# Kernel tuning notes

Measured on AMD Instinct MI355X. Metric: run time of the kernel, lower is better.

The kernel has to match this reference:

```python
import jax, jax.numpy as jnp
import numpy as np

B, D, V, E = 8192, 512, 64, 8
HIDDEN = (1024, 512, 256)


def _mlp_dims(d_in, d_out):
    dims = (d_in,) + HIDDEN + (d_out,)
    return list(zip(dims[:-1], dims[1:]))


def setup_inputs() -> dict:
    key = jax.random.key(0)
    ks = iter(jax.random.split(key, 64))
    inp = {
        'obs': jax.random.normal(next(ks), (B, D), dtype=jnp.float32),
        'code': jax.random.normal(next(ks), (B, V), dtype=jnp.float32),
    }
    # stacked expert MLP params: [E, d_in, d_out] / [E, d_out]
    for i, (di, do) in enumerate(_mlp_dims(D, 1)):
        s = 1.0 / np.sqrt(di)
        inp[f'ew{i}'] = jax.random.uniform(next(ks), (E, di, do), jnp.float32, -s, s)
        inp[f'eb{i}'] = jax.random.uniform(next(ks), (E, do), jnp.float32, -s, s)
    # gate MLP params: [d_in, d_out] / [d_out]
    for i, (di, do) in enumerate(_mlp_dims(V, E)):
        s = 1.0 / np.sqrt(di)
        inp[f'gw{i}'] = jax.random.uniform(next(ks), (di, do), jnp.float32, -s, s)
        inp[f'gb{i}'] = jax.random.uniform(next(ks), (do,), jnp.float32, -s, s)
    return inp


def reference(obs, code, ew0, eb0, ew1, eb1, ew2, eb2, ew3, eb3,
              gw0, gb0, gw1, gb1, gw2, gb2, gw3, gb3):
    # gate: MLP(num_vqvae -> hidden -> num_experts) + softmax
    g = code
    for w, b in ((gw0, gb0), (gw1, gb1), (gw2, gb2)):
        g = jax.nn.elu(g @ w + b)
    weights = jax.nn.softmax(g @ gw3 + gb3, axis=-1)  # [B, E]

    # experts: batched over E via einsum (replaces Python loop of 8 MLPs)
    h = obs  # [B, D] broadcast into [B, E, h]
    h = jax.nn.elu(jnp.einsum('bi,eio->beo', h, ew0) + eb0)
    h = jax.nn.elu(jnp.einsum('bei,eio->beo', h, ew1) + eb1)
    h = jax.nn.elu(jnp.einsum('bei,eio->beo', h, ew2) + eb2)
    returns = (jnp.einsum('bei,eio->beo', h, ew3) + eb3)[..., 0]  # [B, E]

    # bmm(weights[B,1,E], returns[B,E,1]).squeeze(-1) -> [B, 1]
    return jnp.sum(weights * returns, axis=-1, keepdims=True)
```

## Files before the change

### kernel.cpp

```cpp
#include <hip/hip_runtime.h>
#include <hip/hip_bf16.h>
#include <math.h>


typedef _Float16 f16x8 __attribute__((ext_vector_type(8)));
typedef float f32x4 __attribute__((ext_vector_type(4)));

#define AS1 __attribute__((address_space(1)))
#define AS3 __attribute__((address_space(3)))
#define SCHED0 __builtin_amdgcn_sched_barrier(0)
#define SBAR __builtin_amdgcn_s_barrier()

__device__ __forceinline__ ushort h2u(_Float16 h){
  union { _Float16 h; ushort u; } v; v.h = h; return v.u;
}
__device__ __forceinline__ float elu_f(float x){
  return x > 0.f ? x : __expf(x) - 1.f;
}

struct AJob { const float* X; ushort* A; int total; };
__global__ void prep_act_all(AJob j0, AJob j1, int t0){
  int i = blockIdx.x * 256 + threadIdx.x;
  AJob J; int idx;
  if (i < t0){ J = j0; idx = i; }
  else { J = j1; idx = i - t0; if (idx >= J.total) return; }
  J.A[idx] = h2u((_Float16)J.X[idx]);
}

struct WJob { const float* W; ushort* Bt; int K, N, nb, nk, blkStart; };
struct WJobs { WJob j[6]; int njobs; };
__global__ void prep_w_all(WJobs jobs){
  __shared__ float tile[32][33];
  int b = blockIdx.x;
  int ji = 0;
  while (ji + 1 < jobs.njobs && b >= jobs.j[ji + 1].blkStart) ji++;
  WJob J = jobs.j[ji];
  int rem = b - J.blkStart;
  int x = rem % J.nb; rem /= J.nb;
  int y = rem % J.nk; int e = rem / J.nk;
  const float* w = J.W + (size_t)e * J.K * J.N;
  ushort* bt = J.Bt + (size_t)e * J.N * J.K;
  int n0 = x * 32, k0 = y * 32;
  for (int i = threadIdx.y; i < 32; i += 8)
    tile[i][threadIdx.x] = w[(size_t)(k0 + i) * J.N + n0 + threadIdx.x];
  __syncthreads();
  for (int jj = threadIdx.y; jj < 32; jj += 8){
    float v = tile[threadIdx.x][jj];
    bt[(size_t)(n0 + jj) * J.K + k0 + threadIdx.x] = h2u((_Float16)v);
  }
}

struct Slice {
  const ushort* A; const ushort* Bt; const float* bias; void* C;
  const float* w3; const float* rbp; float* ret;
  int N, K, log2gx, mode, blkStart, eidx;
};
struct SliceArr { Slice s[9]; int nz; };

__global__ __launch_bounds__(256, 3) void gemm8p(SliceArr args){
  __shared__ __align__(16) ushort As[128][64];
  __shared__ __align__(16) ushort Bs[128][64];
  __shared__ float red[2][128];

  const int nwg  = gridDim.x;
  const int orig = blockIdx.x;
  const int wg   = (orig & 7) * (nwg >> 3) + (orig >> 3);

  int z = 0;
  while (z + 1 < args.nz && wg >= args.s[z + 1].blkStart) z++;
  const Slice sl = args.s[z];
  const int rem = wg - sl.blkStart;
  const int gxm = (1 << sl.log2gx) - 1;
  const int bx  = rem & gxm;
  const int by  = rem >> sl.log2gx;

  const ushort* __restrict__ Ag = sl.A;
  const ushort* __restrict__ Bg = sl.Bt;
  const int K = sl.K;

  const int tid  = threadIdx.x;
  const int lane = tid & 63;
  const int wave = tid >> 6;
  const int wr = wave >> 1;
  const int wc = wave & 1;
  const int rowBase = by * 128;
  const int colBase = bx * 128;
  const int KB = K >> 6;
  const int lr = lane & 15;
  const int lk = (lane >> 4) << 3;
  const int swzR = (lr & 7) << 3;

  const int rS = tid >> 3;
  const int cS = ((tid & 7) << 3) ^ ((rS & 7) << 3);

  auto stage = [&](int kt){
    int tt = (kt < KB) ? kt : (KB - 1);
    int kc = (tt << 6) + cS;
    {
      char* lb = (char*)&As[0][0];
      #pragma unroll
      for (int j = 0; j < 4; j++){
        const ushort* src = Ag + (size_t)(rowBase + j * 32 + rS) * (size_t)K + kc;
        __builtin_amdgcn_global_load_lds((const AS1 void*)src,
                                         (AS3 void*)(lb + j * 4096 + tid * 16), 16, 0, 0);
      }
    }
    {
      char* lb = (char*)&Bs[0][0];
      #pragma unroll
      for (int j = 0; j < 4; j++){
        const ushort* src = Bg + (size_t)(colBase + j * 32 + rS) * (size_t)K + kc;
        __builtin_amdgcn_global_load_lds((const AS1 void*)src,
                                         (AS3 void*)(lb + j * 4096 + tid * 16), 16, 0, 0);
      }
    }
  };

  f16x8 av[4], bv[4];
  auto readKs = [&](int ks){
    int kc = (ks << 5) + lk;
    #pragma unroll
    for (int n = 0; n < 4; n++)
      bv[n] = *(const f16x8*)&Bs[wc * 64 + n * 16 + lr][kc ^ swzR];
    #pragma unroll
    for (int m = 0; m < 4; m++)
      av[m] = *(const f16x8*)&As[wr * 64 + m * 16 + lr][kc ^ swzR];
  };

  f32x4 acc[4][4];
  #pragma unroll
  for (int m = 0; m < 4; m++)
    #pragma unroll
    for (int n = 0; n < 4; n++)
      acc[m][n] = (f32x4){0.f, 0.f, 0.f, 0.f};

  auto mfmaC = [&](){
    #pragma unroll
    for (int m = 0; m < 4; m++)
      #pragma unroll
      for (int n = 0; n < 4; n++)
        acc[m][n] = __builtin_amdgcn_mfma_f32_16x16x32_f16(av[m], bv[n], acc[m][n], 0, 0, 0);
  };

  stage(0);

  for (int t = 0; t < KB; ++t){
    asm volatile("s_waitcnt vmcnt(0)" ::: "memory");
    SCHED0; SBAR; SCHED0;
    readKs(0);
    asm volatile("s_waitcnt lgkmcnt(0)" ::: "memory"); SCHED0;
    __builtin_amdgcn_s_setprio(1); mfmaC(); __builtin_amdgcn_s_setprio(0);
    SCHED0;
    readKs(1);
    asm volatile("s_waitcnt lgkmcnt(0)" ::: "memory"); SCHED0;
    SBAR; SCHED0;
    stage(t + 1); SCHED0;
    __builtin_amdgcn_s_setprio(1); mfmaC(); __builtin_amdgcn_s_setprio(0);
    SCHED0;
  }
  asm volatile("s_waitcnt vmcnt(0)" ::: "memory");

  if (sl.mode == 2){
    __syncthreads();
    #pragma unroll
    for (int m = 0; m < 4; m++){
      float p4[4] = {0.f, 0.f, 0.f, 0.f};
      #pragma unroll
      for (int n = 0; n < 4; n++){
        int col = colBase + wc * 64 + n * 16 + lr;
        float bv2 = sl.bias[col];
        float wv = sl.w3[col];
        #pragma unroll
        for (int r = 0; r < 4; r++)
          p4[r] += elu_f(acc[m][n][r] + bv2) * wv;
      }
      #pragma unroll
      for (int r = 0; r < 4; r++){
        #pragma unroll
        for (int s = 8; s > 0; s >>= 1) p4[r] += __shfl_xor(p4[r], s, 64);
      }
      if ((lane & 15) == 0){
        int hig = lane >> 4;
        int rowoff = wr * 64 + m * 16 + hig * 4;
        #pragma unroll
        for (int r = 0; r < 4; r++)
          red[wc][rowoff + r] = p4[r];
      }
    }
    __syncthreads();
    if (tid < 128){
      float s2 = red[0][tid] + red[1][tid];
      sl.ret[((size_t)bx * 8192 + rowBase + tid) * 8 + sl.eidx] = s2;
    }
    return;
  }

  const int N = sl.N;
  #pragma unroll
  for (int m = 0; m < 4; m++){
    int row0 = rowBase + wr * 64 + m * 16 + ((lane >> 4) << 2);
    #pragma unroll
    for (int n = 0; n < 4; n++){
      int col = colBase + wc * 64 + n * 16 + lr;
      float bv2 = sl.bias[col];
      float v0 = elu_f(acc[m][n][0] + bv2);
      float v1 = elu_f(acc[m][n][1] + bv2);
      float v2 = elu_f(acc[m][n][2] + bv2);
      float v3 = elu_f(acc[m][n][3] + bv2);
      if (sl.mode == 0){
        ushort* C = (ushort*)sl.C;
        size_t r0b = (size_t)row0 * N + col;
        C[r0b]         = h2u((_Float16)v0);
        C[r0b + N]     = h2u((_Float16)v1);
        C[r0b + 2 * N] = h2u((_Float16)v2);
        C[r0b + 3 * N] = h2u((_Float16)v3);
      } else {
        float* C = (float*)sl.C;
        size_t r0b = (size_t)row0 * N + col;
        C[r0b]         = v0;
        C[r0b + N]     = v1;
        C[r0b + 2 * N] = v2;
        C[r0b + 3 * N] = v3;
      }
    }
  }
}

__global__ void gate3_softmax(const float* __restrict__ g2, const float* __restrict__ gw3,
                              const float* __restrict__ gb3, float* __restrict__ wts){
  int row = blockIdx.x * 4 + (threadIdx.x >> 6);
  int lane = threadIdx.x & 63;
  const float* g = g2 + (size_t)row * 256;
  float p[8];
  #pragma unroll
  for (int j = 0; j < 8; j++) p[j] = 0.f;
  for (int k = lane; k < 256; k += 64){
    float x = g[k];
    #pragma unroll
    for (int j = 0; j < 8; j++) p[j] += x * gw3[k * 8 + j];
  }
  #pragma unroll
  for (int j = 0; j < 8; j++){
    #pragma unroll
    for (int s = 32; s > 0; s >>= 1) p[j] += __shfl_xor(p[j], s, 64);
  }
  float mx = -1e30f;
  #pragma unroll
  for (int j = 0; j < 8; j++){ p[j] += gb3[j]; mx = fmaxf(mx, p[j]); }
  float sum = 0.f;
  #pragma unroll
  for (int j = 0; j < 8; j++){ p[j] = expf(p[j] - mx); sum += p[j]; }
  float inv = 1.f / sum;
  #pragma unroll
  for (int j = 0; j < 8; j++)
    if (lane == j) wts[(size_t)row * 8 + j] = p[j] * inv;
}

__global__ void combine(const float* __restrict__ wts, const float* __restrict__ ret2,
                        const float* __restrict__ eb3, float* __restrict__ out){
  int i = blockIdx.x * blockDim.x + threadIdx.x;
  if (i >= 8192) return;
  float s = 0.f;
  #pragma unroll
  for (int j = 0; j < 8; j++){
    float r = ret2[(size_t)i * 8 + j] + ret2[65536 + (size_t)i * 8 + j] + eb3[j];
    s += wts[(size_t)i * 8 + j] * r;
  }
  out[i] = s;
}

extern "C" void kernel_launch(void* const* d_in, const int* in_sizes, int n_in,
                              void* d_out, int out_size, void* d_ws, size_t ws_size,
                              hipStream_t stream){
  const float* obs  = (const float*)d_in[0];
  const float* code = (const float*)d_in[1];
  const float* ew0  = (const float*)d_in[2];
  const float* eb0  = (const float*)d_in[3];
  const float* ew1  = (const float*)d_in[4];
  const float* eb1  = (const float*)d_in[5];
  const float* ew2  = (const float*)d_in[6];
  const float* eb2  = (const float*)d_in[7];
  const float* ew3  = (const float*)d_in[8];
  const float* eb3  = (const float*)d_in[9];
  const float* gw0  = (const float*)d_in[10];
  const float* gb0  = (const float*)d_in[11];
  const float* gw1  = (const float*)d_in[12];
  const float* gb1  = (const float*)d_in[13];
  const float* gw2  = (const float*)d_in[14];
  const float* gb2  = (const float*)d_in[15];
  const float* gw3  = (const float*)d_in[16];
  const float* gb3  = (const float*)d_in[17];
  (void)in_sizes; (void)n_in; (void)out_size;

  char* ws = (char*)d_ws;
  size_t off = 0;
  auto alloc = [&](size_t bytes) -> void* {
    void* p = ws + off;
    off += (bytes + 255) & ~(size_t)255;
    return p;
  };
  ushort* A_obs  = (ushort*)alloc(8192ull * 512 * 2);
  ushort* A_code = (ushort*)alloc(8192ull * 64 * 2);
  ushort* B_ew0  = (ushort*)alloc(8ull * 1024 * 512 * 2);
  ushort* B_ew1  = (ushort*)alloc(8ull * 512 * 1024 * 2);
  ushort* B_ew2  = (ushort*)alloc(8ull * 256 * 512 * 2);
  ushort* B_gw0  = (ushort*)alloc(1024ull * 64 * 2);
  ushort* B_gw1  = (ushort*)alloc(512ull * 1024 * 2);
  ushort* B_gw2  = (ushort*)alloc(256ull * 512 * 2);
  float*  wts    = (float*)alloc(8192ull * 8 * 4);
  float*  ret2   = (float*)alloc(2ull * 8192 * 8 * 4);
  const size_t fixed = off;

  const size_t sl0b = 8192ull * 1024 * 2;
  const size_t sl1b = 8192ull * 512 * 2;
  const size_t pairB = sl0b + sl1b;

  int G = 0;
  {
    const int cand[5] = {8, 4, 3, 2, 1};
    for (int ci = 0; ci < 5; ci++)
      if (fixed + (size_t)(cand[ci] + 1) * pairB <= ws_size){ G = cand[ci]; break; }
  }
  const bool gateFirst = (G == 0);
  const int ns = gateFirst ? 1 : (G + 1);
  ushort* h0buf = (ushort*)alloc((size_t)ns * sl0b);
  ushort* h1buf = (ushort*)alloc((size_t)ns * sl1b);
  const size_t sl0e = 8192ull * 1024;
  const size_t sl1e = 8192ull * 512;
  const int gsl = ns - 1;
  ushort* h0g = h0buf + (size_t)gsl * sl0e;
  ushort* h1g = h1buf + (size_t)gsl * sl1e;
  float*  h2g = (float*)h0g;

  {
    AJob j0 = {obs,  A_obs,  8192 * 512};
    AJob j1 = {code, A_code, 8192 * 64};
    int t0 = 8192 * 512;
    prep_act_all<<<dim3((t0 + j1.total + 255) / 256), 256, 0, stream>>>(j0, j1, t0);

    WJobs wj; wj.njobs = 6;
    int bs = 0;
    auto addW = [&](int i, const float* W, ushort* Bt, int K, int N, int E){
      wj.j[i] = {W, Bt, K, N, N / 32, K / 32, bs};
      bs += E * (N / 32) * (K / 32);
    };
    addW(0, ew0, B_ew0, 512, 1024, 8);
    addW(1, ew1, B_ew1, 1024, 512, 8);
    addW(2, ew2, B_ew2, 512, 256, 8);
    addW(3, gw0, B_gw0, 64, 1024, 1);
    addW(4, gw1, B_gw1, 1024, 512, 1);
    addW(5, gw2, B_gw2, 512, 256, 1);
    prep_w_all<<<dim3(bs), dim3(32, 8), 0, stream>>>(wj);
  }

  const int NB0 = 8 * 64;
  const int NB1 = 4 * 64;
  const int NB2 = 2 * 64;

  auto runGroup = [&](int e0, int cnt, bool withGate){
    SliceArr sa; int nb;
    nb = 0; sa.nz = cnt + (withGate ? 1 : 0);
    for (int i = 0; i < cnt; i++){ int e = e0 + i;
      sa.s[i] = {A_obs, B_ew0 + (size_t)e * 1024 * 512, eb0 + e * 1024,
                 h0buf + (size_t)i * sl0e, nullptr, nullptr, nullptr,
                 1024, 512, 3, 0, nb, 0};
      nb += NB0;
    }
    if (withGate){
      sa.s[cnt] = {A_code, B_gw0, gb0, h0g, nullptr, nullptr, nullptr,
                   1024, 64, 3, 0, nb, 0};
      nb += NB0;
    }
    for (int i = sa.nz; i < 9; i++) sa.s[i] = sa.s[0];
    gemm8p<<<dim3(nb), 256, 0, stream>>>(sa);
    nb = 0;
    for (int i = 0; i < cnt; i++){ int e = e0 + i;
      sa.s[i] = {h0buf + (size_t)i * sl0e, B_ew1 + (size_t)e * 512 * 1024, eb1 + e * 512,
                 h1buf + (size_t)i * sl1e, nullptr, nullptr, nullptr,
                 512, 1024, 2, 0, nb, 0};
      nb += NB1;
    }
    if (withGate){
      sa.s[cnt] = {h0g, B_gw1, gb1, h1g, nullptr, nullptr, nullptr,
                   512, 1024, 2, 0, nb, 0};
      nb += NB1;
    }
    gemm8p<<<dim3(nb), 256, 0, stream>>>(sa);
    nb = 0;
    for (int i = 0; i < cnt; i++){ int e = e0 + i;
      sa.s[i] = {h1buf + (size_t)i * sl1e, B_ew2 + (size_t)e * 256 * 512, eb2 + e * 256,
                 nullptr, ew3 + (size_t)e * 256, eb3 + e, ret2,
                 256, 512, 1, 2, nb, e};
      nb += NB2;
    }
    if (withGate){
      sa.s[cnt] = {h1g, B_gw2, gb2, h2g, nullptr, nullptr, nullptr,
                   256, 512, 1, 1, nb, 0};
      nb += NB2;
    }
    gemm8p<<<dim3(nb), 256, 0, stream>>>(sa);
    if (withGate)
      gate3_softmax<<<dim3(2048), 256, 0, stream>>>(h2g, gw3, gb3, wts);
  };

  if (gateFirst){
    SliceArr sa; sa.nz = 1;
    sa.s[0] = {A_code, B_gw0, gb0, h0g, nullptr, nullptr, nullptr, 1024, 64, 3, 0, 0, 0};
    for (int i = 1; i < 9; i++) sa.s[i] = sa.s[0];
    gemm8p<<<dim3(NB0), 256, 0, stream>>>(sa);
    sa.s[0] = {h0g, B_gw1, gb1, h1g, nullptr, nullptr, nullptr, 512, 1024, 2, 0, 0, 0};
    gemm8p<<<dim3(NB1), 256, 0, stream>>>(sa);
    sa.s[0] = {h1g, B_gw2, gb2, h2g, nullptr, nullptr, nullptr, 256, 512, 1, 1, 0, 0};
    gemm8p<<<dim3(NB2), 256, 0, stream>>>(sa);
    gate3_softmax<<<dim3(2048), 256, 0, stream>>>(h2g, gw3, gb3, wts);
    for (int e = 0; e < 8; e++) runGroup(e, 1, false);
  } else {
    bool first = true;
    for (int e0 = 0; e0 < 8; ){
      int cnt = (8 - e0 < G) ? (8 - e0) : G;
      runGroup(e0, cnt, first);
      first = false;
      e0 += cnt;
    }
  }

  combine<<<dim3(8192 / 256), 256, 0, stream>>>(wts, ret2, eb3, (float*)d_out);
}
```

Measured before the change: 287.1 us.

## Transpose MFMA output for vectorized epilogue stores and fuse gate softmax with combine

The MFMA operands are swapped so that each lane holds four consecutive columns of one row. The epilogue can then load bias and w3 as float4 and write fp16 or fp32 results with a single vector store instead of four strided scalar stores. The mode-2 reduction needs fewer shuffles. The final gate softmax and the combine kernel are merged into one launch, which removes the weights buffer round trip and one kernel launch. The fused kernel does the softmax and combine on a single lane per row, which serializes that part.

```diff
diff --git a/kernel.cpp b/kernel.cpp
--- a/kernel.cpp
+++ b/kernel.cpp
@@ -5,6 +5,7 @@
 
 typedef _Float16 f16x8 __attribute__((ext_vector_type(8)));
 typedef float f32x4 __attribute__((ext_vector_type(4)));
+typedef ushort ushort4v __attribute__((ext_vector_type(4)));
 
 #define AS1 __attribute__((address_space(1)))
 #define AS3 __attribute__((address_space(3)))
@@ -139,7 +140,7 @@
     for (int m = 0; m < 4; m++)
       #pragma unroll
       for (int n = 0; n < 4; n++)
-        acc[m][n] = __builtin_amdgcn_mfma_f32_16x16x32_f16(av[m], bv[n], acc[m][n], 0, 0, 0);
+        acc[m][n] = __builtin_amdgcn_mfma_f32_16x16x32_f16(bv[n], av[m], acc[m][n], 0, 0, 0);
   };
 
   stage(0);
@@ -160,32 +161,27 @@
   }
   asm volatile("s_waitcnt vmcnt(0)" ::: "memory");
 
+  const int rowL = lane & 15;
+  const int c4  = (lane >> 4) << 2;
+
   if (sl.mode == 2){
     __syncthreads();
     #pragma unroll
     for (int m = 0; m < 4; m++){
-      float p4[4] = {0.f, 0.f, 0.f, 0.f};
+      float s = 0.f;
       #pragma unroll
       for (int n = 0; n < 4; n++){
-        int col = colBase + wc * 64 + n * 16 + lr;
-        float bv2 = sl.bias[col];
-        float wv = sl.w3[col];
+        int col0 = colBase + wc * 64 + n * 16 + c4;
+        f32x4 bv4 = *(const f32x4*)&sl.bias[col0];
+        f32x4 wv4 = *(const f32x4*)&sl.w3[col0];
         #pragma unroll
         for (int r = 0; r < 4; r++)
-          p4[r] += elu_f(acc[m][n][r] + bv2) * wv;
+          s += elu_f(acc[m][n][r] + bv4[r]) * wv4[r];
       }
-      #pragma unroll
-      for (int r = 0; r < 4; r++){
-        #pragma unroll
-        for (int s = 8; s > 0; s >>= 1) p4[r] += __shfl_xor(p4[r], s, 64);
-      }
-      if ((lane & 15) == 0){
-        int hig = lane >> 4;
-        int rowoff = wr * 64 + m * 16 + hig * 4;
-        #pragma unroll
-        for (int r = 0; r < 4; r++)
-          red[wc][rowoff + r] = p4[r];
-      }
+      s += __shfl_xor(s, 16, 64);
+      s += __shfl_xor(s, 32, 64);
+      if (lane < 16)
+        red[wc][wr * 64 + m * 16 + rowL] = s;
     }
     __syncthreads();
     if (tid < 128){
@@ -198,36 +194,30 @@
   const int N = sl.N;
   #pragma unroll
   for (int m = 0; m < 4; m++){
-    int row0 = rowBase + wr * 64 + m * 16 + ((lane >> 4) << 2);
+    int row = rowBase + wr * 64 + m * 16 + rowL;
     #pragma unroll
     for (int n = 0; n < 4; n++){
-      int col = colBase + wc * 64 + n * 16 + lr;
-      float bv2 = sl.bias[col];
-      float v0 = elu_f(acc[m][n][0] + bv2);
-      float v1 = elu_f(acc[m][n][1] + bv2);
-      float v2 = elu_f(acc[m][n][2] + bv2);
-      float v3 = elu_f(acc[m][n][3] + bv2);
+      int col0 = colBase + wc * 64 + n * 16 + c4;
+      f32x4 bv4 = *(const f32x4*)&sl.bias[col0];
+      float v0 = elu_f(acc[m][n][0] + bv4[0]);
+      float v1 = elu_f(acc[m][n][1] + bv4[1]);
+      float v2 = elu_f(acc[m][n][2] + bv4[2]);
+      float v3 = elu_f(acc[m][n][3] + bv4[3]);
       if (sl.mode == 0){
-        ushort* C = (ushort*)sl.C;
-        size_t r0b = (size_t)row0 * N + col;
-        C[r0b]         = h2u((_Float16)v0);
-        C[r0b + N]     = h2u((_Float16)v1);
-        C[r0b + 2 * N] = h2u((_Float16)v2);
-        C[r0b + 3 * N] = h2u((_Float16)v3);
+        ushort4v pk = { h2u((_Float16)v0), h2u((_Float16)v1),
+                        h2u((_Float16)v2), h2u((_Float16)v3) };
+        *(ushort4v*)((ushort*)sl.C + (size_t)row * N + col0) = pk;
       } else {
-        float* C = (float*)sl.C;
-        size_t r0b = (size_t)row0 * N + col;
-        C[r0b]         = v0;
-        C[r0b + N]     = v1;
-        C[r0b + 2 * N] = v2;
-        C[r0b + 3 * N] = v3;
+        f32x4 pv = { v0, v1, v2, v3 };
+        *(f32x4*)((float*)sl.C + (size_t)row * N + col0) = pv;
       }
     }
   }
 }
 
-__global__ void gate3_softmax(const float* __restrict__ g2, const float* __restrict__ gw3,
-                              const float* __restrict__ gb3, float* __restrict__ wts){
+__global__ void gate3_combine(const float* __restrict__ g2, const float* __restrict__ gw3,
+                              const float* __restrict__ gb3, const float* __restrict__ ret2,
+                              const float* __restrict__ eb3, float* __restrict__ out){
   int row = blockIdx.x * 4 + (threadIdx.x >> 6);
   int lane = threadIdx.x & 63;
   const float* g = g2 + (size_t)row * 256;
@@ -244,29 +234,22 @@
     #pragma unroll
     for (int s = 32; s > 0; s >>= 1) p[j] += __shfl_xor(p[j], s, 64);
   }
-  float mx = -1e30f;
-  #pragma unroll
-  for (int j = 0; j < 8; j++){ p[j] += gb3[j]; mx = fmaxf(mx, p[j]); }
-  float sum = 0.f;
-  #pragma unroll
-  for (int j = 0; j < 8; j++){ p[j] = expf(p[j] - mx); sum += p[j]; }
-  float inv = 1.f / sum;
-  #pragma unroll
-  for (int j = 0; j < 8; j++)
-    if (lane == j) wts[(size_t)row * 8 + j] = p[j] * inv;
-}
-
-__global__ void combine(const float* __restrict__ wts, const float* __restrict__ ret2,
-                        const float* __restrict__ eb3, float* __restrict__ out){
-  int i = blockIdx.x * blockDim.x + threadIdx.x;
-  if (i >= 8192) return;
-  float s = 0.f;
-  #pragma unroll
-  for (int j = 0; j < 8; j++){
-    float r = ret2[(size_t)i * 8 + j] + ret2[65536 + (size_t)i * 8 + j] + eb3[j];
-    s += wts[(size_t)i * 8 + j] * r;
-  }
-  out[i] = s;
+  if (lane == 0){
+    float mx = -1e30f;
+    #pragma unroll
+    for (int j = 0; j < 8; j++){ p[j] += gb3[j]; mx = fmaxf(mx, p[j]); }
+    float sum = 0.f;
+    #pragma unroll
+    for (int j = 0; j < 8; j++){ p[j] = expf(p[j] - mx); sum += p[j]; }
+    float inv = 1.f / sum;
+    float s = 0.f;
+    #pragma unroll
+    for (int j = 0; j < 8; j++){
+      float r = ret2[(size_t)row * 8 + j] + ret2[65536 + (size_t)row * 8 + j] + eb3[j];
+      s += p[j] * inv * r;
+    }
+    out[row] = s;
+  }
 }
 
 extern "C" void kernel_launch(void* const* d_in, const int* in_sizes, int n_in,
@@ -307,7 +290,6 @@
   ushort* B_gw0  = (ushort*)alloc(1024ull * 64 * 2);
   ushort* B_gw1  = (ushort*)alloc(512ull * 1024 * 2);
   ushort* B_gw2  = (ushort*)alloc(256ull * 512 * 2);
-  float*  wts    = (float*)alloc(8192ull * 8 * 4);
   float*  ret2   = (float*)alloc(2ull * 8192 * 8 * 4);
   const size_t fixed = off;
 
@@ -399,8 +381,6 @@
       nb += NB2;
     }
     gemm8p<<<dim3(nb), 256, 0, stream>>>(sa);
-    if (withGate)
-      gate3_softmax<<<dim3(2048), 256, 0, stream>>>(h2g, gw3, gb3, wts);
   };
 
   if (gateFirst){
@@ -412,7 +392,6 @@
     gemm8p<<<dim3(NB1), 256, 0, stream>>>(sa);
     sa.s[0] = {h1g, B_gw2, gb2, h2g, nullptr, nullptr, nullptr, 256, 512, 1, 1, 0, 0};
     gemm8p<<<dim3(NB2), 256, 0, stream>>>(sa);
-    gate3_softmax<<<dim3(2048), 256, 0, stream>>>(h2g, gw3, gb3, wts);
     for (int e = 0; e < 8; e++) runGroup(e, 1, false);
   } else {
     bool first = true;
@@ -424,5 +403,5 @@
     }
   }
 
-  combine<<<dim3(8192 / 256), 256, 0, stream>>>(wts, ret2, eb3, (float*)d_out);
-}
+  gate3_combine<<<dim3(2048), 256, 0, stream>>>(h2g, gw3, gb3, ret2, eb3, (float*)d_out);
+}
```

Measured after the change: 302.6 us. 1.05x slower.
